# Performance work log

Measured on AMD Instinct MI355X. Metric: run time of the kernel, lower is better.

The kernel has to match this reference:

```python
import jax, jax.numpy as jnp
import numpy as np

B, NDOCK, DCELL, C, H, W, HD = 65536, 3, 25, 32, 8, 8, 16


def setup_inputs() -> dict:
    key = jax.random.key(0)
    ks = jax.random.split(key, 10)
    s_q = 1.0 / np.sqrt(DCELL)
    s_kv = 1.0 / np.sqrt(C)
    s_o = 1.0 / np.sqrt(HD)
    return {
        "dock_masks": jax.random.uniform(ks[0], (B, NDOCK, DCELL), dtype=jnp.float32),
        "grid_feat": jax.random.normal(ks[1], (B, C, H, W), dtype=jnp.float32),
        "Wq": jax.random.uniform(ks[2], (HD, DCELL), jnp.float32, -s_q, s_q),
        "bq": jax.random.uniform(ks[3], (HD,), jnp.float32, -s_q, s_q),
        "Wk": jax.random.uniform(ks[4], (HD, C), jnp.float32, -s_kv, s_kv),  # conv1x1 kernel squeezed
        "bk": jax.random.uniform(ks[5], (HD,), jnp.float32, -s_kv, s_kv),
        "Wv": jax.random.uniform(ks[6], (HD, C), jnp.float32, -s_kv, s_kv),
        "bv": jax.random.uniform(ks[7], (HD,), jnp.float32, -s_kv, s_kv),
        "Wo": jax.random.uniform(ks[8], (HD, HD), jnp.float32, -s_o, s_o),
        "bo": jax.random.uniform(ks[9], (HD,), jnp.float32, -s_o, s_o),
    }


def reference(dock_masks, grid_feat, Wq, bq, Wk, bk, Wv, bv, Wo, bo):
    b = dock_masks.shape[0]
    hd = Wq.shape[0]
    # Q: [B, 3, hd]
    q = jnp.einsum("bnc,dc->bnd", dock_masks, Wq) + bq
    # K, V via 1x1 conv == channel matmul: [B, hd, H*W]
    g = grid_feat.reshape(b, grid_feat.shape[1], -1)  # [B, C, HW]
    k = jnp.einsum("bcs,dc->bds", g, Wk) + bk[None, :, None]
    v = jnp.einsum("bcs,dc->bds", g, Wv) + bv[None, :, None]
    # attention: [B, 3, HW]
    attn = jax.nn.softmax(jnp.einsum("bnd,bds->bns", q, k) / jnp.sqrt(jnp.float32(hd)), axis=-1)
    # context: [B, 3, hd]
    ctx = jnp.einsum("bns,bds->bnd", attn, v)
    out = jnp.einsum("bnd,ed->bne", ctx, Wo) + bo
    return out.reshape(b, -1)
```

## Files before the change

kernel.cpp:

```cpp
#include <hip/hip_runtime.h>


#define NW 4

__global__ void precompute_kernel(const float* __restrict__ Wq, const float* __restrict__ bq,
                                  const float* __restrict__ Wk, const float* __restrict__ Wv,
                                  const float* __restrict__ bv, const float* __restrict__ Wo,
                                  const float* __restrict__ bo, float* __restrict__ ws)
{
    const float K = 0.25f * 1.44269504088896f;
    const int t = threadIdx.x;
    for (int i = t; i < 800; i += 256) {
        int j = i >> 5, c = i & 31;
        float s = 0.f;
        #pragma unroll
        for (int d = 0; d < 16; ++d) s += Wq[d * 25 + j] * Wk[d * 32 + c];
        ws[i] = s * K;
    }
    if (t < 32) {
        float s = 0.f;
        #pragma unroll
        for (int d = 0; d < 16; ++d) s += bq[d] * Wk[d * 32 + t];
        ws[800 + t] = s * K;
    }
    for (int i = t; i < 512; i += 256) {
        int e = i >> 5, c = i & 31;
        float s = 0.f;
        #pragma unroll
        for (int d = 0; d < 16; ++d) s += Wo[e * 16 + d] * Wv[d * 32 + c];
        ws[832 + i] = s;
    }
    if (t < 16) {
        float s = bo[t];
        #pragma unroll
        for (int d = 0; d < 16; ++d) s += Wo[t * 16 + d] * bv[d];
        ws[1344 + t] = s;
    }
}

__device__ __forceinline__ float rl(float v, int srclane) {
    return __int_as_float(__builtin_amdgcn_readlane(__float_as_int(v), srclane));
}

__device__ __forceinline__ void gload_lds16(const float* src, float* dst_lds) {
    __builtin_amdgcn_global_load_lds(
        (const __attribute__((address_space(1))) void*)src,
        (__attribute__((address_space(3))) void*)dst_lds, 16, 0, 0);
}

__global__ __launch_bounds__(256, 4) void dock_attn_kernel(
    const float* __restrict__ dock,
    const float* __restrict__ grid,
    const float* __restrict__ ws,
    float* __restrict__ out,
    int b_total)
{
    __shared__ __align__(16) float gT[NW][2048];
    __shared__ __align__(16) float AL[NW][96];
    __shared__ __align__(16) float attnL[NW][192];
    __shared__ __align__(16) float zL[NW][104];

    const int tid = threadIdx.x;
    const int w = tid >> 6, lane = tid & 63;
    const int b = blockIdx.x * NW + w;
    if (b >= b_total) return;

    const float* Mg  = ws;
    const float* bkt = ws + 800;
    const float* Ug  = ws + 832;
    const float* c0  = ws + 1344;

    float mreg[25];
    float bi = 0.f;
    if (lane < 32) {
        #pragma unroll
        for (int j = 0; j < 25; ++j) mreg[j] = Mg[j * 32 + lane];
        bi = bkt[lane];
    }
    float d0 = dock[(size_t)b * 75 + lane];
    float d1 = (lane < 11) ? dock[(size_t)b * 75 + 64 + lane] : 0.f;

    asm volatile("" ::: "memory");

    {
        const float* gb = grid + (size_t)b * 2048;
        const int h = lane >> 4, q = lane & 15;
        #pragma unroll
        for (int i = 0; i < 8; ++i) {
            const int c = 4 * i + h;
            const int s4 = q ^ (c & 15);
            gload_lds16(gb + c * 64 + 4 * s4, &gT[w][i * 256]);
        }
    }

    if (lane < 32) {
        float a0 = bi, a1 = bi, a2 = bi;
        #pragma unroll
        for (int j = 0; j < 25; ++j) {
            float m = mreg[j];
            float q0 = rl(d0, j);
            float q1 = rl(d0, 25 + j);
            float q2 = (50 + j < 64) ? rl(d0, 50 + j) : rl(d1, 50 + j - 64);
            a0 = fmaf(q0, m, a0);
            a1 = fmaf(q1, m, a1);
            a2 = fmaf(q2, m, a2);
        }
        AL[w][lane] = a0; AL[w][32 + lane] = a1; AL[w][64 + lane] = a2;
    }

    asm volatile("s_waitcnt vmcnt(0)" ::: "memory");

    float sc0 = 0.f, sc1 = 0.f, sc2 = 0.f;
    {
        const float* gTw = &gT[w][0];
        const float4* A4 = (const float4*)&AL[w][0];
        #pragma unroll
        for (int qq = 0; qq < 8; ++qq) {
            float4 a = A4[qq], bb = A4[8 + qq], cc = A4[16 + qq];
            const int c = 4 * qq;
            float g0 = gTw[((c + 0) << 6) + (lane ^ (((c + 0) & 15) << 2))];
            float g1 = gTw[((c + 1) << 6) + (lane ^ (((c + 1) & 15) << 2))];
            float g2 = gTw[((c + 2) << 6) + (lane ^ (((c + 2) & 15) << 2))];
            float g3 = gTw[((c + 3) << 6) + (lane ^ (((c + 3) & 15) << 2))];
            sc0 = fmaf(a.x, g0, fmaf(a.y, g1, fmaf(a.z, g2, fmaf(a.w, g3, sc0))));
            sc1 = fmaf(bb.x, g0, fmaf(bb.y, g1, fmaf(bb.z, g2, fmaf(bb.w, g3, sc1))));
            sc2 = fmaf(cc.x, g0, fmaf(cc.y, g1, fmaf(cc.z, g2, fmaf(cc.w, g3, sc2))));
        }
    }

    attnL[w][lane]       = exp2f(sc0);
    attnL[w][64 + lane]  = exp2f(sc1);
    attnL[w][128 + lane] = exp2f(sc2);

    {
        const int n = lane >> 5, c = lane & 31, cx = c & 15;
        const float4* ar = (const float4*)&attnL[w][n * 64];
        const float* grow = &gT[w][c << 6];
        float ax = 0.f, ay = 0.f, az = 0.f, aw = 0.f;
        #pragma unroll
        for (int j = 0; j < 16; ++j) {
            float4 a  = ar[j];
            float4 gg = *(const float4*)&grow[(j ^ cx) << 2];
            ax = fmaf(a.x, gg.x, ax);
            ay = fmaf(a.y, gg.y, ay);
            az = fmaf(a.z, gg.z, az);
            aw = fmaf(a.w, gg.w, aw);
        }
        zL[w][n * 32 + c] = (ax + ay) + (az + aw);
    }
    if (lane < 32) {
        const int cx = lane & 15;
        const float4* ar = (const float4*)&attnL[w][128];
        const float* grow = &gT[w][lane << 6];
        float ax = 0.f, ay = 0.f, az = 0.f, aw = 0.f;
        #pragma unroll
        for (int j = 0; j < 16; ++j) {
            float4 a  = ar[j];
            float4 gg = *(const float4*)&grow[(j ^ cx) << 2];
            ax = fmaf(a.x, gg.x, ax);
            ay = fmaf(a.y, gg.y, ay);
            az = fmaf(a.z, gg.z, az);
            aw = fmaf(a.w, gg.w, aw);
        }
        zL[w][64 + lane] = (ax + ay) + (az + aw);
    } else if (lane < 35) {
        const float4* ar = (const float4*)&attnL[w][(lane - 32) * 64];
        float s0 = 0.f, s1 = 0.f, s2 = 0.f, s3 = 0.f;
        #pragma unroll
        for (int j = 0; j < 16; ++j) {
            float4 a = ar[j];
            s0 += a.x; s1 += a.y; s2 += a.z; s3 += a.w;
        }
        zL[w][96 + (lane - 32)] = (s0 + s1) + (s2 + s3);
    }

    if (lane < 48) {
        const int n = lane >> 4, e = lane & 15;
        const float4* Ur = (const float4*)(Ug + e * 32);
        const float4* zr = (const float4*)&zL[w][n * 32];
        float dinv = __builtin_amdgcn_rcpf(zL[w][96 + n]);
        float acc0 = 0.f, acc1 = 0.f, acc2 = 0.f, acc3 = 0.f;
        #pragma unroll
        for (int qq = 0; qq < 8; ++qq) {
            float4 u = Ur[qq], z = zr[qq];
            acc0 = fmaf(u.x, z.x, acc0);
            acc1 = fmaf(u.y, z.y, acc1);
            acc2 = fmaf(u.z, z.z, acc2);
            acc3 = fmaf(u.w, z.w, acc3);
        }
        out[(size_t)b * 48 + lane] = fmaf((acc0 + acc1) + (acc2 + acc3), dinv, c0[e]);
    }
}

extern "C" void kernel_launch(void* const* d_in, const int* in_sizes, int n_in,
                              void* d_out, int out_size, void* d_ws, size_t ws_size,
                              hipStream_t stream) {
    const float* dock = (const float*)d_in[0];
    const float* grid = (const float*)d_in[1];
    const float* Wq   = (const float*)d_in[2];
    const float* bq   = (const float*)d_in[3];
    const float* Wk   = (const float*)d_in[4];
    const float* Wv   = (const float*)d_in[6];
    const float* bv   = (const float*)d_in[7];
    const float* Wo   = (const float*)d_in[8];
    const float* bo   = (const float*)d_in[9];
    float* out = (float*)d_out;
    float* ws  = (float*)d_ws;

    precompute_kernel<<<1, 256, 0, stream>>>(Wq, bq, Wk, Wv, bv, Wo, bo, ws);

    const int b_total = in_sizes[0] / 75;
    const int blocks = (b_total + NW - 1) / NW;
    dock_attn_kernel<<<blocks, 256, 0, stream>>>(dock, grid, ws, out, b_total);
}
```

Measured before the change: 715.2 us.

## Process two batches per wavefront with overlapped grid loads

Each wavefront now handles two consecutive batch items. It issues async global-to-LDS loads for both grids up front, then waits on only the first set (vmcnt(8)) before computing the first item while the second load is still in flight. The Mg weight registers and dock loads are amortised across two items. LDS per block doubles and launch_bounds drops to 2 blocks per CU, which lowers occupancy. There is also no guard for b0+1 exceeding b_total when the batch count is odd.

```diff
diff --git a/kernel.cpp b/kernel.cpp
--- a/kernel.cpp
+++ b/kernel.cpp
@@ -48,72 +48,17 @@
         (__attribute__((address_space(3))) void*)dst_lds, 16, 0, 0);
 }
 
-__global__ __launch_bounds__(256, 4) void dock_attn_kernel(
-    const float* __restrict__ dock,
-    const float* __restrict__ grid,
-    const float* __restrict__ ws,
-    float* __restrict__ out,
-    int b_total)
+__device__ __forceinline__ float batch_compute(const float* __restrict__ gTw,
+                                               const float* __restrict__ ALw,
+                                               float* __restrict__ attnLw,
+                                               float* __restrict__ zLw,
+                                               const float* __restrict__ Ug,
+                                               const float* __restrict__ c0,
+                                               int lane)
 {
-    __shared__ __align__(16) float gT[NW][2048];
-    __shared__ __align__(16) float AL[NW][96];
-    __shared__ __align__(16) float attnL[NW][192];
-    __shared__ __align__(16) float zL[NW][104];
-
-    const int tid = threadIdx.x;
-    const int w = tid >> 6, lane = tid & 63;
-    const int b = blockIdx.x * NW + w;
-    if (b >= b_total) return;
-
-    const float* Mg  = ws;
-    const float* bkt = ws + 800;
-    const float* Ug  = ws + 832;
-    const float* c0  = ws + 1344;
-
-    float mreg[25];
-    float bi = 0.f;
-    if (lane < 32) {
-        #pragma unroll
-        for (int j = 0; j < 25; ++j) mreg[j] = Mg[j * 32 + lane];
-        bi = bkt[lane];
-    }
-    float d0 = dock[(size_t)b * 75 + lane];
-    float d1 = (lane < 11) ? dock[(size_t)b * 75 + 64 + lane] : 0.f;
-
-    asm volatile("" ::: "memory");
-
-    {
-        const float* gb = grid + (size_t)b * 2048;
-        const int h = lane >> 4, q = lane & 15;
-        #pragma unroll
-        for (int i = 0; i < 8; ++i) {
-            const int c = 4 * i + h;
-            const int s4 = q ^ (c & 15);
-            gload_lds16(gb + c * 64 + 4 * s4, &gT[w][i * 256]);
-        }
-    }
-
-    if (lane < 32) {
-        float a0 = bi, a1 = bi, a2 = bi;
-        #pragma unroll
-        for (int j = 0; j < 25; ++j) {
-            float m = mreg[j];
-            float q0 = rl(d0, j);
-            float q1 = rl(d0, 25 + j);
-            float q2 = (50 + j < 64) ? rl(d0, 50 + j) : rl(d1, 50 + j - 64);
-            a0 = fmaf(q0, m, a0);
-            a1 = fmaf(q1, m, a1);
-            a2 = fmaf(q2, m, a2);
-        }
-        AL[w][lane] = a0; AL[w][32 + lane] = a1; AL[w][64 + lane] = a2;
-    }
-
-    asm volatile("s_waitcnt vmcnt(0)" ::: "memory");
-
     float sc0 = 0.f, sc1 = 0.f, sc2 = 0.f;
     {
-        const float* gTw = &gT[w][0];
-        const float4* A4 = (const float4*)&AL[w][0];
+        const float4* A4 = (const float4*)ALw;
         #pragma unroll
         for (int qq = 0; qq < 8; ++qq) {
             float4 a = A4[qq], bb = A4[8 + qq], cc = A4[16 + qq];
@@ -128,14 +73,14 @@
         }
     }
 
-    attnL[w][lane]       = exp2f(sc0);
-    attnL[w][64 + lane]  = exp2f(sc1);
-    attnL[w][128 + lane] = exp2f(sc2);
+    attnLw[lane]       = exp2f(sc0);
+    attnLw[64 + lane]  = exp2f(sc1);
+    attnLw[128 + lane] = exp2f(sc2);
 
     {
         const int n = lane >> 5, c = lane & 31, cx = c & 15;
-        const float4* ar = (const float4*)&attnL[w][n * 64];
-        const float* grow = &gT[w][c << 6];
+        const float4* ar = (const float4*)&attnLw[n * 64];
+        const float* grow = &gTw[c << 6];
         float ax = 0.f, ay = 0.f, az = 0.f, aw = 0.f;
         #pragma unroll
         for (int j = 0; j < 16; ++j) {
@@ -146,12 +91,12 @@
             az = fmaf(a.z, gg.z, az);
             aw = fmaf(a.w, gg.w, aw);
         }
-        zL[w][n * 32 + c] = (ax + ay) + (az + aw);
+        zLw[n * 32 + c] = (ax + ay) + (az + aw);
     }
     if (lane < 32) {
         const int cx = lane & 15;
-        const float4* ar = (const float4*)&attnL[w][128];
-        const float* grow = &gT[w][lane << 6];
+        const float4* ar = (const float4*)&attnLw[128];
+        const float* grow = &gTw[lane << 6];
         float ax = 0.f, ay = 0.f, az = 0.f, aw = 0.f;
         #pragma unroll
         for (int j = 0; j < 16; ++j) {
@@ -162,23 +107,24 @@
             az = fmaf(a.z, gg.z, az);
             aw = fmaf(a.w, gg.w, aw);
         }
-        zL[w][64 + lane] = (ax + ay) + (az + aw);
+        zLw[64 + lane] = (ax + ay) + (az + aw);
     } else if (lane < 35) {
-        const float4* ar = (const float4*)&attnL[w][(lane - 32) * 64];
+        const float4* ar = (const float4*)&attnLw[(lane - 32) * 64];
         float s0 = 0.f, s1 = 0.f, s2 = 0.f, s3 = 0.f;
         #pragma unroll
         for (int j = 0; j < 16; ++j) {
             float4 a = ar[j];
             s0 += a.x; s1 += a.y; s2 += a.z; s3 += a.w;
         }
-        zL[w][96 + (lane - 32)] = (s0 + s1) + (s2 + s3);
-    }
-
+        zLw[96 + (lane - 32)] = (s0 + s1) + (s2 + s3);
+    }
+
+    float o = 0.f;
     if (lane < 48) {
         const int n = lane >> 4, e = lane & 15;
         const float4* Ur = (const float4*)(Ug + e * 32);
-        const float4* zr = (const float4*)&zL[w][n * 32];
-        float dinv = __builtin_amdgcn_rcpf(zL[w][96 + n]);
+        const float4* zr = (const float4*)&zLw[n * 32];
+        float dinv = __builtin_amdgcn_rcpf(zLw[96 + n]);
         float acc0 = 0.f, acc1 = 0.f, acc2 = 0.f, acc3 = 0.f;
         #pragma unroll
         for (int qq = 0; qq < 8; ++qq) {
@@ -188,8 +134,95 @@
             acc2 = fmaf(u.z, z.z, acc2);
             acc3 = fmaf(u.w, z.w, acc3);
         }
-        out[(size_t)b * 48 + lane] = fmaf((acc0 + acc1) + (acc2 + acc3), dinv, c0[e]);
-    }
+        o = fmaf((acc0 + acc1) + (acc2 + acc3), dinv, c0[e]);
+    }
+    return o;
+}
+
+__global__ __launch_bounds__(256, 2) void dock_attn_kernel(
+    const float* __restrict__ dock,
+    const float* __restrict__ grid,
+    const float* __restrict__ ws,
+    float* __restrict__ out,
+    int b_total)
+{
+    __shared__ __align__(16) float gT[NW][2][2048];
+    __shared__ __align__(16) float AL[NW][2][96];
+    __shared__ __align__(16) float attnL[NW][192];
+    __shared__ __align__(16) float zL[NW][104];
+
+    const int tid = threadIdx.x;
+    const int w = tid >> 6, lane = tid & 63;
+    const int b0 = (blockIdx.x * NW + w) * 2;
+    if (b0 >= b_total) return;
+
+    const float* Mg  = ws;
+    const float* bkt = ws + 800;
+    const float* Ug  = ws + 832;
+    const float* c0  = ws + 1344;
+
+    float mreg[25];
+    float bi = 0.f;
+    if (lane < 32) {
+        #pragma unroll
+        for (int j = 0; j < 25; ++j) mreg[j] = Mg[j * 32 + lane];
+        bi = bkt[lane];
+    }
+    const float* dkb = dock + (size_t)b0 * 75;
+    float e0 = dkb[lane];
+    float e1 = dkb[64 + lane];
+    float e2 = (lane < 22) ? dkb[128 + lane] : 0.f;
+
+    asm volatile("" ::: "memory");
+
+    {
+        const float* gb0 = grid + (size_t)b0 * 2048;
+        const int h = lane >> 4, q = lane & 15;
+        #pragma unroll
+        for (int i = 0; i < 8; ++i) {
+            const int c = 4 * i + h;
+            const int s4 = q ^ (c & 15);
+            gload_lds16(gb0 + c * 64 + 4 * s4, &gT[w][0][i * 256]);
+        }
+        #pragma unroll
+        for (int i = 0; i < 8; ++i) {
+            const int c = 4 * i + h;
+            const int s4 = q ^ (c & 15);
+            gload_lds16(gb0 + 2048 + c * 64 + 4 * s4, &gT[w][1][i * 256]);
+        }
+    }
+
+    if (lane < 32) {
+        float a0 = bi, a1 = bi, a2 = bi;
+        float b0a = bi, b1a = bi, b2a = bi;
+        #pragma unroll
+        for (int j = 0; j < 25; ++j) {
+            float m = mreg[j];
+            float q0 = rl(e0, j);
+            float q1 = rl(e0, 25 + j);
+            float q2 = (j < 14) ? rl(e0, 50 + j) : rl(e1, j - 14);
+            a0 = fmaf(q0, m, a0);
+            a1 = fmaf(q1, m, a1);
+            a2 = fmaf(q2, m, a2);
+            float p0 = rl(e1, 11 + j);
+            float p1 = rl(e1, 36 + j);
+            float p2 = (j < 3) ? rl(e1, 61 + j) : rl(e2, j - 3);
+            b0a = fmaf(p0, m, b0a);
+            b1a = fmaf(p1, m, b1a);
+            b2a = fmaf(p2, m, b2a);
+        }
+        AL[w][0][lane] = a0; AL[w][0][32 + lane] = a1; AL[w][0][64 + lane] = a2;
+        AL[w][1][lane] = b0a; AL[w][1][32 + lane] = b1a; AL[w][1][64 + lane] = b2a;
+    }
+
+    asm volatile("s_waitcnt vmcnt(8)" ::: "memory");
+    float o0 = batch_compute(&gT[w][0][0], &AL[w][0][0], attnL[w], zL[w], Ug, c0, lane);
+
+    asm volatile("s_waitcnt vmcnt(0)" ::: "memory");
+    if (lane < 48) out[(size_t)b0 * 48 + lane] = o0;
+
+    float o1 = batch_compute(&gT[w][1][0], &AL[w][1][0], attnL[w], zL[w], Ug, c0, lane);
+    if (lane < 48) out[(size_t)(b0 + 1) * 48 + lane] = o1;
 }
 
 extern "C" void kernel_launch(void* const* d_in, const int* in_sizes, int n_in,
@@ -210,6 +243,6 @@
     precompute_kernel<<<1, 256, 0, stream>>>(Wq, bq, Wk, Wv, bv, Wo, bo, ws);
 
     const int b_total = in_sizes[0] / 75;
-    const int blocks = (b_total + NW - 1) / NW;
+    const int blocks = (b_total + 2 * NW - 1) / (2 * NW);
     dock_attn_kernel<<<blocks, 256, 0, stream>>>(dock, grid, ws, out, b_total);
 }
```

Result: slower. 739.7 us (+3.4%).

## Load grid tile into registers and stage half-tiles through smaller LDS

Applied to the files above, without the earlier changes.

Replaces the async global-to-LDS load of the whole 32x64 grid tile with direct coalesced register loads of 32 values per lane. The score pass now reads registers instead of swizzled LDS, and the context pass writes the tile to LDS in two 16-channel halves, halving LDS per wave. Launch bounds are raised to target 6 blocks per CU. The mask weight registers are dropped and read from global inside the loop. This aims at higher occupancy and less LDS traffic, at the cost of 32 live registers per lane, extra LDS write passes and the loss of overlap between the async load and the Q projection.

```diff
diff --git a/kernel.cpp b/kernel.cpp
--- a/kernel.cpp
+++ b/kernel.cpp
@@ -42,20 +42,14 @@
     return __int_as_float(__builtin_amdgcn_readlane(__float_as_int(v), srclane));
 }
 
-__device__ __forceinline__ void gload_lds16(const float* src, float* dst_lds) {
-    __builtin_amdgcn_global_load_lds(
-        (const __attribute__((address_space(1))) void*)src,
-        (__attribute__((address_space(3))) void*)dst_lds, 16, 0, 0);
-}
-
-__global__ __launch_bounds__(256, 4) void dock_attn_kernel(
+__global__ __launch_bounds__(256, 6) void dock_attn_kernel(
     const float* __restrict__ dock,
     const float* __restrict__ grid,
     const float* __restrict__ ws,
     float* __restrict__ out,
     int b_total)
 {
-    __shared__ __align__(16) float gT[NW][2048];
+    __shared__ __align__(16) float gH[NW][1024];
     __shared__ __align__(16) float AL[NW][96];
     __shared__ __align__(16) float attnL[NW][192];
     __shared__ __align__(16) float zL[NW][104];
@@ -70,34 +64,20 @@
     const float* Ug  = ws + 832;
     const float* c0  = ws + 1344;
 
-    float mreg[25];
-    float bi = 0.f;
-    if (lane < 32) {
-        #pragma unroll
-        for (int j = 0; j < 25; ++j) mreg[j] = Mg[j * 32 + lane];
-        bi = bkt[lane];
-    }
+    const float* gp = grid + (size_t)b * 2048 + lane;
+    float g[32];
+    #pragma unroll
+    for (int c = 0; c < 32; ++c) g[c] = gp[c * 64];
+
     float d0 = dock[(size_t)b * 75 + lane];
     float d1 = (lane < 11) ? dock[(size_t)b * 75 + 64 + lane] : 0.f;
 
-    asm volatile("" ::: "memory");
-
-    {
-        const float* gb = grid + (size_t)b * 2048;
-        const int h = lane >> 4, q = lane & 15;
-        #pragma unroll
-        for (int i = 0; i < 8; ++i) {
-            const int c = 4 * i + h;
-            const int s4 = q ^ (c & 15);
-            gload_lds16(gb + c * 64 + 4 * s4, &gT[w][i * 256]);
-        }
-    }
-
     if (lane < 32) {
+        float bi = bkt[lane];
         float a0 = bi, a1 = bi, a2 = bi;
         #pragma unroll
         for (int j = 0; j < 25; ++j) {
-            float m = mreg[j];
+            float m = Mg[j * 32 + lane];
             float q0 = rl(d0, j);
             float q1 = rl(d0, 25 + j);
             float q2 = (50 + j < 64) ? rl(d0, 50 + j) : rl(d1, 50 + j - 64);
@@ -108,20 +88,13 @@
         AL[w][lane] = a0; AL[w][32 + lane] = a1; AL[w][64 + lane] = a2;
     }
 
-    asm volatile("s_waitcnt vmcnt(0)" ::: "memory");
-
     float sc0 = 0.f, sc1 = 0.f, sc2 = 0.f;
     {
-        const float* gTw = &gT[w][0];
         const float4* A4 = (const float4*)&AL[w][0];
         #pragma unroll
         for (int qq = 0; qq < 8; ++qq) {
             float4 a = A4[qq], bb = A4[8 + qq], cc = A4[16 + qq];
-            const int c = 4 * qq;
-            float g0 = gTw[((c + 0) << 6) + (lane ^ (((c + 0) & 15) << 2))];
-            float g1 = gTw[((c + 1) << 6) + (lane ^ (((c + 1) & 15) << 2))];
-            float g2 = gTw[((c + 2) << 6) + (lane ^ (((c + 2) & 15) << 2))];
-            float g3 = gTw[((c + 3) << 6) + (lane ^ (((c + 3) & 15) << 2))];
+            float g0 = g[4 * qq], g1 = g[4 * qq + 1], g2 = g[4 * qq + 2], g3 = g[4 * qq + 3];
             sc0 = fmaf(a.x, g0, fmaf(a.y, g1, fmaf(a.z, g2, fmaf(a.w, g3, sc0))));
             sc1 = fmaf(bb.x, g0, fmaf(bb.y, g1, fmaf(bb.z, g2, fmaf(bb.w, g3, sc1))));
             sc2 = fmaf(cc.x, g0, fmaf(cc.y, g1, fmaf(cc.z, g2, fmaf(cc.w, g3, sc2))));
@@ -132,46 +105,58 @@
     attnL[w][64 + lane]  = exp2f(sc1);
     attnL[w][128 + lane] = exp2f(sc2);
 
-    {
-        const int n = lane >> 5, c = lane & 31, cx = c & 15;
+    #pragma unroll
+    for (int c = 0; c < 16; ++c)
+        gH[w][(c << 6) + ((((lane >> 2) ^ c) << 2) | (lane & 3))] = g[c];
+
+    if (lane < 48) {
+        const int n = lane >> 4, r = lane & 15;
         const float4* ar = (const float4*)&attnL[w][n * 64];
-        const float* grow = &gT[w][c << 6];
+        const float* grow = &gH[w][r << 6];
         float ax = 0.f, ay = 0.f, az = 0.f, aw = 0.f;
         #pragma unroll
         for (int j = 0; j < 16; ++j) {
             float4 a  = ar[j];
-            float4 gg = *(const float4*)&grow[(j ^ cx) << 2];
+            float4 gg = *(const float4*)&grow[(j ^ r) << 2];
             ax = fmaf(a.x, gg.x, ax);
             ay = fmaf(a.y, gg.y, ay);
             az = fmaf(a.z, gg.z, az);
             aw = fmaf(a.w, gg.w, aw);
         }
-        zL[w][n * 32 + c] = (ax + ay) + (az + aw);
-    }
-    if (lane < 32) {
-        const int cx = lane & 15;
-        const float4* ar = (const float4*)&attnL[w][128];
-        const float* grow = &gT[w][lane << 6];
+        zL[w][n * 32 + r] = (ax + ay) + (az + aw);
+    } else if (lane < 51) {
+        const int n = lane - 48;
+        const float4* ar = (const float4*)&attnL[w][n * 64];
+        float s0 = 0.f, s1 = 0.f, s2 = 0.f, s3 = 0.f;
+        #pragma unroll
+        for (int j = 0; j < 16; ++j) {
+            float4 a = ar[j];
+            s0 += a.x; s1 += a.y; s2 += a.z; s3 += a.w;
+        }
+        zL[w][96 + n] = (s0 + s1) + (s2 + s3);
+    }
+
+    #pragma unroll
+    for (int c = 16; c < 32; ++c) {
+        const int r = c - 16;
+        gH[w][(r << 6) + ((((lane >> 2) ^ r) << 2) | (lane & 3))] = g[c];
+    }
+
+    if (lane < 48) {
+        const int n = lane >> 4, r = lane & 15;
+        const float4* ar = (const float4*)&attnL[w][n * 64];
+        const float* grow = &gH[w][r << 6];
         float ax = 0.f, ay = 0.f, az = 0.f, aw = 0.f;
         #pragma unroll
         for (int j = 0; j < 16; ++j) {
             float4 a  = ar[j];
-            float4 gg = *(const float4*)&grow[(j ^ cx) << 2];
+            float4 gg = *(const float4*)&grow[(j ^ r) << 2];
             ax = fmaf(a.x, gg.x, ax);
             ay = fmaf(a.y, gg.y, ay);
             az = fmaf(a.z, gg.z, az);
             aw = fmaf(a.w, gg.w, aw);
         }
-        zL[w][64 + lane] = (ax + ay) + (az + aw);
-    } else if (lane < 35) {
-        const float4* ar = (const float4*)&attnL[w][(lane - 32) * 64];
-        float s0 = 0.f, s1 = 0.f, s2 = 0.f, s3 = 0.f;
-        #pragma unroll
-        for (int j = 0; j < 16; ++j) {
-            float4 a = ar[j];
-            s0 += a.x; s1 += a.y; s2 += a.z; s3 += a.w;
-        }
-        zL[w][96 + (lane - 32)] = (s0 + s1) + (s2 + s3);
+        zL[w][n * 32 + 16 + r] = (ax + ay) + (az + aw);
     }
 
     if (lane < 48) {
```

Result: slower. 744.2 us (+4.1%).
